# Optimization experiments

Measured on AMD Instinct MI355X. Metric: run time of the kernel, lower is better.

## Reference

```python
import jax, jax.numpy as jnp
import numpy as np
from jax import lax

# dims: B batch, V views, D feature dim, C classes, P prompts
B, V, D, C, P = 512, 10, 1024, 100, 4
ADAPTER_RATIO = 0.6
EPS = 0.01          # sinkhorn entropic regularizer (compute_logits default)
MAX_ITER = 1000     # compute_logits default
THRESH = 1e-2       # PLOT Sinkhorn early-stop threshold on |r - r_prev|.mean()
BN_EPS = 1e-5


def setup_inputs() -> dict:
    key = jax.random.key(0)
    ks = jax.random.split(key, 8)
    # Correlated features so cosine similarity ~0.9 (realistic CLIP-like sims);
    # keeps exp(-wdist/0.01) well inside fp32 range for the Sinkhorn solver.
    base = jax.random.normal(ks[0], (D,), jnp.float32)
    feat = base[None, :] + 0.3 * jax.random.normal(ks[1], (B * V, D), jnp.float32)
    text_feat = base[None, None, :] + 0.3 * jax.random.normal(ks[2], (C, P, D), jnp.float32)
    w = lambda k, shp: 0.02 * jax.random.normal(k, shp, jnp.float32)
    return {
        "feat": feat,                       # (B*V, D) CLIP visual features
        "text_feat": text_feat,             # (C, P, D) encoded text features
        "fusion_ratio": jnp.full((V,), 0.5, jnp.float32),
        "bn1_gamma": jnp.ones((D,), jnp.float32),
        "bn1_beta": jnp.zeros((D,), jnp.float32),
        "W_glob": w(ks[3], (D, D * V)),     # Linear(D*V -> D), torch layout (out, in)
        "b_glob": jnp.zeros((D,), jnp.float32),
        "bn2_gamma": jnp.ones((D,), jnp.float32),
        "bn2_beta": jnp.zeros((D,), jnp.float32),
        "W_v1": w(ks[4], (D, D)),           # Linear(D -> D)
        "b_v1": jnp.zeros((D,), jnp.float32),
        "W_v2": w(ks[5], (D * V, D)),       # Linear(D -> D*V)
        "b_v2": jnp.zeros((D * V,), jnp.float32),
        "logit_scale": jnp.array(np.log(1.0 / 0.07), jnp.float32),
    }


def _bn_train(x, gamma, beta):
    # BatchNorm1d in training mode: biased batch statistics over axis 0
    m = x.mean(axis=0)
    v = x.var(axis=0)
    return (x - m) * lax.rsqrt(v + BN_EPS) * gamma + beta


def _adapter(feat, fusion_ratio, bn1_g, bn1_b, Wg, bg, bn2_g, bn2_b, Wv1, bv1, Wv2, bv2):
    img = feat.reshape(-1, V, D)
    res = feat.reshape(-1, V * D)
    x = img * fusion_ratio.reshape(1, -1, 1)          # per-view fusion weights
    x = _bn_train(x.reshape(-1, D), bn1_g, bn1_b)     # BatchNormPoint over D
    x = x.reshape(-1, V * D)                          # Flatten
    g = jax.nn.relu(_bn_train(x @ Wg.T + bg, bn2_g, bn2_b))   # global_f (dropout=0)
    view = jax.nn.relu(jax.nn.relu(g @ Wv1.T + bv1) @ Wv2.T + bv2)  # view_f
    return view * ADAPTER_RATIO + res * (1.0 - ADAPTER_RATIO)


def _sinkhorn(K, p, q):
    # PLOT-style Sinkhorn: r = p / (K c); c = q / (K^T r); early stop on mean |dr|
    r0 = jnp.ones_like(p)
    c0 = jnp.ones_like(q)

    def cond(st):
        i, r, c, err = st
        return jnp.logical_and(i < MAX_ITER, err > THRESH)

    def body(st):
        i, r, c, _ = st
        r_prev = r
        r = p / jnp.einsum('nvp,np->nv', K, c)
        c = q / jnp.einsum('nvp,nv->np', K, r)
        err = jnp.mean(jnp.abs(r - r_prev))
        return i + 1, r, c, err

    _, r, c, _ = lax.while_loop(cond, body, (jnp.int32(0), r0, c0, jnp.float32(jnp.inf)))
    return r[:, :, None] * K * c[:, None, :]   # T = diag(r) K diag(c)


def reference(feat, text_feat, fusion_ratio, bn1_gamma, bn1_beta, W_glob, b_glob,
              bn2_gamma, bn2_beta, W_v1, b_v1, W_v2, b_v2, logit_scale):
    img_feat = _adapter(feat, fusion_ratio, bn1_gamma, bn1_beta, W_glob, b_glob,
                        bn2_gamma, bn2_beta, W_v1, b_v1, W_v2, b_v2)
    img_feat = img_feat.reshape(-1, V, D)
    img_feat = img_feat / jnp.linalg.norm(img_feat, axis=-1, keepdims=True)
    txt = text_feat / jnp.linalg.norm(text_feat, axis=-1, keepdims=True)

    # compute_logits: sim (B, C, V, P) -> (B*C, V, P)
    sim = jnp.einsum('bvd,cpd->bcvp', img_feat, txt).reshape(B * C, V, P)
    wdist = 1.0 - sim
    p = jnp.full((B * C, V), 1.0 / V, sim.dtype)
    q = jnp.full((B * C, P), 1.0 / P, sim.dtype)
    K = jnp.exp(-wdist / EPS)
    T = _sinkhorn(lax.stop_gradient(K), p, q)   # solver runs under no_grad
    d_OT = jnp.sum(T * wdist, axis=(1, 2)).reshape(B, C)
    logits = jnp.exp(logit_scale) * (1.0 - d_OT)
    return logits
```

## Files before the change

### kernel.cpp

```cpp
#include <hip/hip_runtime.h>
#include <cstdint>


typedef unsigned short u16;
typedef __attribute__((ext_vector_type(8))) short bf8v;
typedef __attribute__((ext_vector_type(4))) float f4v;

__device__ __forceinline__ float4 ld4(const float* p){ return *reinterpret_cast<const float4*>(p); }
__device__ __forceinline__ void st4(float* p, float4 v){ *reinterpret_cast<float4*>(p) = v; }
__device__ __forceinline__ u16 f2bf(float x){
  uint32_t u = __float_as_uint(x);
  return (u16)((u + 0x7FFFu + ((u>>16)&1u)) >> 16);
}
__device__ __forceinline__ uint32_t pk(float a, float b){
  return (uint32_t)f2bf(a) | ((uint32_t)f2bf(b)<<16);
}
__device__ __forceinline__ void glds16(const u16* g, u16* l){
  __builtin_amdgcn_global_load_lds(
      (const __attribute__((address_space(1))) unsigned int*)g,
      (__attribute__((address_space(3))) unsigned int*)l, 16, 0, 0);
}

__device__ __forceinline__ void remap(int map, int NBX, int NBY,
                                      int& bx, int& by, int& bz)
{
  if (map == 0){ bx = blockIdx.x; by = blockIdx.y; bz = blockIdx.z; return; }
  const int i = blockIdx.x, xcd = i & 7, j = i >> 3;
  if (map == 1){
    const int mnC = NBX*NBY;
    const int zPer = (gridDim.x >> 3) / mnC;
    bz = xcd*zPer + j/mnC;
    const int mn = j % mnC; bx = mn % NBX; by = mn / NBX;
  } else {
    const int nbxPer = NBX >> 3;
    bx = xcd*nbxPer + j % nbxPer; by = j / nbxPer; bz = 0;
  }
}

__global__ __launch_bounds__(256,4)
void gemm_bf16_nt(const u16* __restrict__ A, const u16* __restrict__ B,
                  float* __restrict__ C, int lda, int ldb, int ldc,
                  int kLen, long strideCz, int map, int NBX, int NBY)
{
  __shared__ u16 As0[2048], Bs0[4096], As1[2048], Bs1[4096];
  const int tid = threadIdx.x, lane = tid & 63, w = tid >> 6;
  int bx, by, bz; remap(map, NBX, NBY, bx, by, bz);

  const long bm = (long)by*64, bn = (long)bx*128;
  const long kz = (long)bz*kLen;
  C += (long)bz*strideCz;

  const int srow  = lane>>2;
  const int sslot = (lane&3) ^ ((lane>>3)&3);
  const u16* Ag = A + (bm + w*16 + srow)*(long)lda + kz + sslot*8;
  const u16* Bg = B + (bn + w*32 + srow)*(long)ldb + kz + sslot*8;
  const long b16 = 16L*ldb;
  const int woffA = w*512, woffB = w*1024;

  const int fr = lane & 15;
  const int rslot = ((lane>>4) ^ ((lane>>1)&3))*16;
  const int wr = (w>>1)*32, wc = (w&1)*64;

  const f4v zero = {0.f,0.f,0.f,0.f};
  f4v acc[2][4];
  #pragma unroll
  for (int i2=0;i2<2;i2++)
    #pragma unroll
    for (int j2=0;j2<4;j2++) acc[i2][j2]=zero;

  auto STAGE = [&](u16* Al, u16* Bl, int kt){
    glds16(Ag + kt,       Al + woffA);
    glds16(Bg + kt,       Bl + woffB);
    glds16(Bg + kt + b16, Bl + woffB + 512);
  };
  auto COMPUTE = [&](const u16* Asb, const u16* Bsb){
    bf8v af[2], bf[4];
    #pragma unroll
    for (int mi=0; mi<2; ++mi)
      af[mi] = *(const bf8v*)((const char*)Asb + (wr+mi*16+fr)*64 + rslot);
    #pragma unroll
    for (int nj=0; nj<4; ++nj)
      bf[nj] = *(const bf8v*)((const char*)Bsb + (wc+nj*16+fr)*64 + rslot);
    #pragma unroll
    for (int mi=0; mi<2; ++mi)
      #pragma unroll
      for (int nj=0; nj<4; ++nj)
        acc[mi][nj] = __builtin_amdgcn_mfma_f32_16x16x32_bf16(af[mi], bf[nj], acc[mi][nj], 0,0,0);
  };

  STAGE(As0, Bs0, 0);
  __syncthreads();
  int kt = 32;
  for (; kt < kLen - 32; kt += 64){
    STAGE(As1, Bs1, kt);
    COMPUTE(As0, Bs0);
    __syncthreads();
    STAGE(As0, Bs0, kt + 32);
    COMPUTE(As1, Bs1);
    __syncthreads();
  }
  STAGE(As1, Bs1, kt);
  COMPUTE(As0, Bs0);
  __syncthreads();
  COMPUTE(As1, Bs1);

  const int orow = (lane>>4)*4;
  #pragma unroll
  for (int mi=0;mi<2;++mi){
    #pragma unroll
    for (int q=0;q<4;++q){
      const long row = bm + wr + mi*16 + orow + q;
      float* Crow = C + row*(long)ldc + bn + wc + fr;
      #pragma unroll
      for (int nj=0;nj<4;++nj) Crow[nj*16] = acc[mi][nj][q];
    }
  }
}

__global__ __launch_bounds__(256)
void cvt_w(const float* __restrict__ Wg, const float* __restrict__ Wv1,
           u16* __restrict__ WB, u16* __restrict__ W1b)
{
  const long NG = 1310720;
  const long NT = NG + 131072;
  for (long i = (long)blockIdx.x*256 + threadIdx.x; i < NT; i += (long)gridDim.x*256){
    const float* src; u16* dst; long k;
    if (i < NG){ src = Wg; dst = WB; k = i; }
    else       { src = Wv1; dst = W1b; k = i - NG; }
    const float4 a = ld4(&src[k*8]), b = ld4(&src[k*8+4]);
    uint4 o;
    o.x = pk(a.x,a.y); o.y = pk(a.z,a.w);
    o.z = pk(b.x,b.y); o.w = pk(b.z,b.w);
    *reinterpret_cast<uint4*>(&dst[k*8]) = o;
  }
}

__global__ __launch_bounds__(256)
void cvt_bf16(const float* __restrict__ in, u16* __restrict__ out, long n8)
{
  for (long i = (long)blockIdx.x*256 + threadIdx.x; i < n8; i += (long)gridDim.x*256){
    const float4 a = ld4(&in[i*8]), b = ld4(&in[i*8+4]);
    uint4 o;
    o.x = pk(a.x,a.y); o.y = pk(a.z,a.w);
    o.z = pk(b.x,b.y); o.w = pk(b.z,b.w);
    *reinterpret_cast<uint4*>(&out[i*8]) = o;
  }
}

__global__ __launch_bounds__(256)
void reduce_f32_stats(const float* __restrict__ P, int S, int MN,
                      const float* __restrict__ bias, float* __restrict__ out,
                      float* __restrict__ part)
{
  const int b = blockIdx.x, t = threadIdx.x;
  const long i = (long)b*1024 + t*4;
  float4 s = ld4(&P[i]);
  for (int z=1; z<S; ++z){
    const float4 v = ld4(&P[(long)z*MN + i]);
    s.x+=v.x; s.y+=v.y; s.z+=v.z; s.w+=v.w;
  }
  const float4 bb = ld4(&bias[t*4]);
  s.x+=bb.x; s.y+=bb.y; s.z+=bb.z; s.w+=bb.w;
  st4(&out[i], s);
  float* p = part + (long)b*2048;
  st4(&p[t*4], s);
  st4(&p[1024+t*4], make_float4(s.x*s.x, s.y*s.y, s.z*s.z, s.w*s.w));
}

__global__ __launch_bounds__(256)
void reduce_bf16(const float* __restrict__ P, int S, int MN,
                 const float* __restrict__ bias, u16* __restrict__ out)
{
  const long i = ((long)blockIdx.x*256 + threadIdx.x)*4;
  float4 s = ld4(&P[i]);
  for (int z=1; z<S; ++z){
    const float4 v = ld4(&P[(long)z*MN + i]);
    s.x+=v.x; s.y+=v.y; s.z+=v.z; s.w+=v.w;
  }
  const float4 b = ld4(&bias[(int)(i & 1023)]);
  s.x = fmaxf(s.x+b.x,0.f); s.y = fmaxf(s.y+b.y,0.f);
  s.z = fmaxf(s.z+b.z,0.f); s.w = fmaxf(s.w+b.w,0.f);
  uint2 o; o.x = pk(s.x,s.y); o.y = pk(s.z,s.w);
  *reinterpret_cast<uint2*>(&out[i]) = o;
}

__global__ __launch_bounds__(256)
void colstats_p1(const float* __restrict__ X, int rpb, const float* __restrict__ fr,
                 float* __restrict__ part)
{
  const int c = threadIdx.x*4;
  const long r0 = (long)blockIdx.x*rpb;
  float4 s = make_float4(0,0,0,0), q = make_float4(0,0,0,0);
  for (int rr=0; rr<rpb; ++rr){
    const long r = r0+rr;
    float4 x = ld4(&X[r*1024 + c]);
    if (fr){ const float f = fr[(int)(r%10)]; x.x*=f; x.y*=f; x.z*=f; x.w*=f; }
    s.x+=x.x; s.y+=x.y; s.z+=x.z; s.w+=x.w;
    q.x+=x.x*x.x; q.y+=x.y*x.y; q.z+=x.z*x.z; q.w+=x.w*x.w;
  }
  float* p = part + (long)blockIdx.x*2048;
  st4(&p[c], s);
  st4(&p[1024+c], q);
}

__global__ __launch_bounds__(256)
void colstats_reduce(const float* __restrict__ in, float* __restrict__ out,
                     int nslab, int chunk)
{
  const int idx = blockIdx.x*256 + threadIdx.x;
  const int s0 = blockIdx.y*chunk;
  const int s1 = min(nslab, s0+chunk);
  float a0=0.f, a1=0.f, a2=0.f, a3=0.f;
  int s = s0;
  for (; s+4 <= s1; s += 4){
    a0 += in[(long)s*2048+idx];
    a1 += in[(long)(s+1)*2048+idx];
    a2 += in[(long)(s+2)*2048+idx];
    a3 += in[(long)(s+3)*2048+idx];
  }
  for (; s < s1; ++s) a0 += in[(long)s*2048+idx];
  out[(long)blockIdx.y*2048 + idx] = (a0+a1)+(a2+a3);
}

__global__ __launch_bounds__(256)
void bn_apply_bf16(const float* __restrict__ X, const float* __restrict__ fr,
                   const float* __restrict__ stats, float invN,
                   const float* __restrict__ gamma,
                   const float* __restrict__ beta, int relu, u16* __restrict__ out)
{
  const long i = ((long)blockIdx.x*256 + threadIdx.x)*4;
  const int d = (int)(i & 1023);
  const float4 s  = ld4(&stats[d]);
  const float4 qq = ld4(&stats[1024+d]);
  const float4 gm = ld4(&gamma[d]);
  const float4 bt = ld4(&beta[d]);
  float4 sc, sh;
  { const float m=s.x*invN, v=qq.x*invN-m*m; sc.x=gm.x*rsqrtf(v+1e-5f); sh.x=bt.x-m*sc.x; }
  { const float m=s.y*invN, v=qq.y*invN-m*m; sc.y=gm.y*rsqrtf(v+1e-5f); sh.y=bt.y-m*sc.y; }
  { const float m=s.z*invN, v=qq.z*invN-m*m; sc.z=gm.z*rsqrtf(v+1e-5f); sh.z=bt.z-m*sc.z; }
  { const float m=s.w*invN, v=qq.w*invN-m*m; sc.w=gm.w*rsqrtf(v+1e-5f); sh.w=bt.w-m*sc.w; }
  float4 x = ld4(&X[i]);
  if (fr){ const float f = fr[(int)((i>>10)%10)]; x.x*=f; x.y*=f; x.z*=f; x.w*=f; }
  x.x = x.x*sc.x + sh.x; x.y = x.y*sc.y + sh.y;
  x.z = x.z*sc.z + sh.z; x.w = x.w*sc.w + sh.w;
  if (relu){ x.x=fmaxf(x.x,0.f); x.y=fmaxf(x.y,0.f); x.z=fmaxf(x.z,0.f); x.w=fmaxf(x.w,0.f); }
  uint2 o; o.x = pk(x.x,x.y); o.y = pk(x.z,x.w);
  *reinterpret_cast<uint2*>(&out[i]) = o;
}

__device__ __forceinline__ float blockSum256(float v, float* sh4){
  #pragma unroll
  for (int m=32; m; m>>=1) v += __shfl_xor(v, m, 64);
  const int w = threadIdx.x >> 6;
  if ((threadIdx.x & 63) == 0) sh4[w] = v;
  __syncthreads();
  return sh4[0]+sh4[1]+sh4[2]+sh4[3];
}

__global__ __launch_bounds__(256)
void rownorm_bf16(const float* __restrict__ X, u16* __restrict__ out)
{
  __shared__ float sh4[4];
  const int row = blockIdx.x;
  const int d = threadIdx.x*4;
  if (row >= 400){ *reinterpret_cast<uint2*>(&out[(long)row*1024 + d]) = make_uint2(0,0); return; }
  const long base = (long)row*1024 + d;
  const float4 x = ld4(&X[base]);
  const float ss = x.x*x.x + x.y*x.y + x.z*x.z + x.w*x.w;
  const float rn = rsqrtf(blockSum256(ss, sh4));
  uint2 o; o.x = pk(x.x*rn, x.y*rn); o.y = pk(x.z*rn, x.w*rn);
  *reinterpret_cast<uint2*>(&out[base]) = o;
}

__global__ __launch_bounds__(256)
void mix_norm_bf16(const float* __restrict__ P, const float* __restrict__ feat,
                   const float* __restrict__ bv2, u16* __restrict__ outp)
{
  __shared__ float sh4[4];
  const int m = blockIdx.x;
  const int v = m % 10;
  const long base = (long)m*1024;
  const int d = threadIdx.x*4;
  const float4 y  = ld4(&P[base+d]);
  const float4 bb = ld4(&bv2[v*1024 + d]);
  const float4 f  = ld4(&feat[base+d]);
  float4 img;
  img.x = 0.6f*fmaxf(y.x+bb.x,0.f) + 0.4f*f.x;
  img.y = 0.6f*fmaxf(y.y+bb.y,0.f) + 0.4f*f.y;
  img.z = 0.6f*fmaxf(y.z+bb.z,0.f) + 0.4f*f.z;
  img.w = 0.6f*fmaxf(y.w+bb.w,0.f) + 0.4f*f.w;
  const float ss = img.x*img.x + img.y*img.y + img.z*img.z + img.w*img.w;
  const float rn = rsqrtf(blockSum256(ss, sh4));
  uint2 o; o.x = pk(img.x*rn, img.y*rn); o.y = pk(img.z*rn, img.w*rn);
  *reinterpret_cast<uint2*>(&outp[base+d]) = o;
}

__global__ __launch_bounds__(64)
void sinkhorn_solve(const float* __restrict__ sim, const float* __restrict__ lsp,
                    float* __restrict__ out)
{
  const int n = blockIdx.x*64 + threadIdx.x;
  const int b = n / 100, c = n % 100;
  float S[10][4], Km[10][4];
  #pragma unroll
  for (int v=0; v<10; ++v){
    const long off = (long)(b*10+v)*512 + c*4;
    const float4 a0 = ld4(&sim[off]);
    const float4 a1 = ld4(&sim[2621440L + off]);
    S[v][0]=a0.x+a1.x; S[v][1]=a0.y+a1.y; S[v][2]=a0.z+a1.z; S[v][3]=a0.w+a1.w;
    #pragma unroll
    for (int p=0;p<4;++p) Km[v][p] = expf((S[v][p]-1.f)*100.f);
  }
  float r[10], cc[4];
  #pragma unroll
  for (int v=0;v<10;++v) r[v]=1.f;
  #pragma unroll
  for (int p=0;p<4;++p) cc[p]=1.f;
  for (int j=0; j<1000; ++j){
    float lerr = 0.f;
    #pragma unroll
    for (int v=0;v<10;++v){
      const float s = Km[v][0]*cc[0]+Km[v][1]*cc[1]+Km[v][2]*cc[2]+Km[v][3]*cc[3];
      const float rn = __fdividef(0.1f, s);
      lerr += fabsf(rn - r[v]); r[v]=rn;
    }
    #pragma unroll
    for (int p=0;p<4;++p){
      float s = 0.f;
      #pragma unroll
      for (int v=0;v<10;++v) s += Km[v][p]*r[v];
      cc[p] = __fdividef(0.25f, s);
    }
    if (j & 1){
      float w = lerr;
      #pragma unroll
      for (int m=32; m; m>>=1) w += __shfl_xor(w, m, 64);
      if (w <= 0.25f) break;
    }
  }
  float dOT = 0.f;
  #pragma unroll
  for (int v=0;v<10;++v)
    #pragma unroll
    for (int p=0;p<4;++p)
      dOT += r[v]*Km[v][p]*cc[p]*(1.f - S[v][p]);
  out[n] = expf(lsp[0]) * (1.f - dOT);
}

extern "C" void kernel_launch(void* const* d_in, const int* in_sizes, int n_in,
                              void* d_out, int out_size, void* d_ws, size_t ws_size,
                              hipStream_t stream)
{
  const float* feat  = (const float*)d_in[0];
  const float* textf = (const float*)d_in[1];
  const float* fr    = (const float*)d_in[2];
  const float* bn1g  = (const float*)d_in[3];
  const float* bn1b  = (const float*)d_in[4];
  const float* Wg    = (const float*)d_in[5];
  const float* bg    = (const float*)d_in[6];
  const float* bn2g  = (const float*)d_in[7];
  const float* bn2b  = (const float*)d_in[8];
  const float* Wv1   = (const float*)d_in[9];
  const float* bv1   = (const float*)d_in[10];
  const float* Wv2   = (const float*)d_in[11];
  const float* bv2   = (const float*)d_in[12];
  const float* ls    = (const float*)d_in[13];
  float* out = (float*)d_out;
  char* base = (char*)d_ws;

  u16*   WB  = (u16*)(base + 0);
  u16*   Xb  = (u16*)(base + 20971520);
  float* P   = (float*)(base + 31457280);
  float* P2  = P + 1310720;
  u16*   W1b = (u16*)(base + 65011712);
  float* y1  = (float*)(base + 67108864);
  u16*   Gb  = (u16*)(base + 69206016);
  u16*   Hb  = (u16*)(base + 70254592);
  u16*   Tb  = (u16*)(base + 71303168);
  float* ex  = (float*)(base + 72351744);
  float* bn1st=ex, *bn2st=ex+2048;
  float* partY = ex + 4096;
  float* partY2= partY + 1048576;

  cvt_w<<<2048,256,0,stream>>>(Wg, Wv1, WB, W1b);

  colstats_p1<<<640,256,0,stream>>>(feat, 8, fr, P);
  colstats_reduce<<<dim3(8,20),256,0,stream>>>(P, P2, 640, 32);
  colstats_reduce<<<dim3(8,1),256,0,stream>>>(P2, bn1st, 20, 20);
  bn_apply_bf16<<<5120,256,0,stream>>>(feat, fr, bn1st, 1.f/5120.f,
                                       bn1g, bn1b, 0, Xb);

  gemm_bf16_nt<<<1024,256,0,stream>>>(Xb, WB, P, 10240,10240,1024, 640,
                                      524288L, 1, 8, 8);
  reduce_f32_stats<<<512,256,0,stream>>>(P, 16, 524288, bg, y1, partY);
  colstats_reduce<<<dim3(8,16),256,0,stream>>>(partY, partY2, 512, 32);
  colstats_reduce<<<dim3(8,1),256,0,stream>>>(partY2, bn2st, 16, 16);
  bn_apply_bf16<<<512,256,0,stream>>>(y1, nullptr, bn2st, 1.f/512.f,
                                      bn2g, bn2b, 1, Gb);

  gemm_bf16_nt<<<512,256,0,stream>>>(Gb, W1b, P, 1024,1024,1024, 128,
                                     524288L, 1, 8, 8);
  reduce_bf16<<<512,256,0,stream>>>(P, 8, 524288, bv1, Hb);

  cvt_bf16<<<2048,256,0,stream>>>(Wv2, WB, 1310720);

  gemm_bf16_nt<<<640,256,0,stream>>>(Hb, WB, P, 1024,1024,10240, 1024, 0L,
                                     2, 80, 8);
  mix_norm_bf16<<<5120,256,0,stream>>>(P, feat, bv2, Xb);

  rownorm_bf16<<<512,256,0,stream>>>(textf, Tb);
  gemm_bf16_nt<<<dim3(4,80,2),256,0,stream>>>(Xb, Tb, P, 1024,1024,512, 512,
                                              2621440L, 0, 0, 0);

  sinkhorn_solve<<<800,64,0,stream>>>(P, ls, out);
}
```

Baseline: 154.1 us.

## Fuse bias-relu epilogue into GEMM, fold stats reduction, halve split-K

The third GEMM now applies bias, ReLU and the 0.6 scale in its epilogue and writes bf16 directly, so mix_norm reads half the bytes and skips the bias load. The final stat reduction passes are removed by having bn_apply sum 8 partial slabs itself. The big first GEMM's split-K factor drops from 16 to 8, which halves partial-output traffic and the reduce work but also halves grid parallelism. Together these cut several launches and intermediate round-trips. The cost is a little per-thread redundant summation and extra rounding of the intermediate to bf16.

Measured after the change: 167.3 us. +8.6%, slower.

```diff
diff --git a/kernel.cpp b/kernel.cpp
--- a/kernel.cpp
+++ b/kernel.cpp
@@ -12,6 +12,7 @@
   uint32_t u = __float_as_uint(x);
   return (u16)((u + 0x7FFFu + ((u>>16)&1u)) >> 16);
 }
+__device__ __forceinline__ float bf2f(u16 h){ return __uint_as_float(((uint32_t)h)<<16); }
 __device__ __forceinline__ uint32_t pk(float a, float b){
   return (uint32_t)f2bf(a) | ((uint32_t)f2bf(b)<<16);
 }
@@ -40,7 +41,8 @@
 __global__ __launch_bounds__(256,4)
 void gemm_bf16_nt(const u16* __restrict__ A, const u16* __restrict__ B,
                   float* __restrict__ C, int lda, int ldb, int ldc,
-                  int kLen, long strideCz, int map, int NBX, int NBY)
+                  int kLen, long strideCz, int map, int NBX, int NBY,
+                  u16* __restrict__ OB, const float* __restrict__ bv2r)
 {
   __shared__ u16 As0[2048], Bs0[4096], As1[2048], Bs1[4096];
   const int tid = threadIdx.x, lane = tid & 63, w = tid >> 6;
@@ -105,14 +107,31 @@
   COMPUTE(As1, Bs1);
 
   const int orow = (lane>>4)*4;
-  #pragma unroll
-  for (int mi=0;mi<2;++mi){
-    #pragma unroll
-    for (int q=0;q<4;++q){
-      const long row = bm + wr + mi*16 + orow + q;
-      float* Crow = C + row*(long)ldc + bn + wc + fr;
+  if (OB){
+    float bv[4];
+    #pragma unroll
+    for (int nj=0;nj<4;++nj) bv[nj] = bv2r[bn + wc + fr + nj*16];
+    #pragma unroll
+    for (int mi=0;mi<2;++mi){
       #pragma unroll
-      for (int nj=0;nj<4;++nj) Crow[nj*16] = acc[mi][nj][q];
+      for (int q=0;q<4;++q){
+        const long row = bm + wr + mi*16 + orow + q;
+        u16* Orow = OB + row*(long)ldc + bn + wc + fr;
+        #pragma unroll
+        for (int nj=0;nj<4;++nj)
+          Orow[nj*16] = f2bf(0.6f*fmaxf(acc[mi][nj][q] + bv[nj], 0.f));
+      }
+    }
+  } else {
+    #pragma unroll
+    for (int mi=0;mi<2;++mi){
+      #pragma unroll
+      for (int q=0;q<4;++q){
+        const long row = bm + wr + mi*16 + orow + q;
+        float* Crow = C + row*(long)ldc + bn + wc + fr;
+        #pragma unroll
+        for (int nj=0;nj<4;++nj) Crow[nj*16] = acc[mi][nj][q];
+      }
     }
   }
 }
@@ -224,14 +243,19 @@
 
 __global__ __launch_bounds__(256)
 void bn_apply_bf16(const float* __restrict__ X, const float* __restrict__ fr,
-                   const float* __restrict__ stats, float invN,
+                   const float* __restrict__ part, int nslab, float invN,
                    const float* __restrict__ gamma,
                    const float* __restrict__ beta, int relu, u16* __restrict__ out)
 {
   const long i = ((long)blockIdx.x*256 + threadIdx.x)*4;
   const int d = (int)(i & 1023);
-  const float4 s  = ld4(&stats[d]);
-  const float4 qq = ld4(&stats[1024+d]);
+  float4 s = make_float4(0,0,0,0), qq = make_float4(0,0,0,0);
+  for (int sl=0; sl<nslab; ++sl){
+    const float4 a = ld4(&part[(long)sl*2048 + d]);
+    const float4 b = ld4(&part[(long)sl*2048 + 1024 + d]);
+    s.x+=a.x; s.y+=a.y; s.z+=a.z; s.w+=a.w;
+    qq.x+=b.x; qq.y+=b.y; qq.z+=b.z; qq.w+=b.w;
+  }
   const float4 gm = ld4(&gamma[d]);
   const float4 bt = ld4(&beta[d]);
   float4 sc, sh;
@@ -273,22 +297,20 @@
 }
 
 __global__ __launch_bounds__(256)
-void mix_norm_bf16(const float* __restrict__ P, const float* __restrict__ feat,
-                   const float* __restrict__ bv2, u16* __restrict__ outp)
+void mix_norm_bf16(const u16* __restrict__ T3, const float* __restrict__ feat,
+                   u16* __restrict__ outp)
 {
   __shared__ float sh4[4];
   const int m = blockIdx.x;
-  const int v = m % 10;
   const long base = (long)m*1024;
   const int d = threadIdx.x*4;
-  const float4 y  = ld4(&P[base+d]);
-  const float4 bb = ld4(&bv2[v*1024 + d]);
+  const uint2 tv = *reinterpret_cast<const uint2*>(&T3[base+d]);
   const float4 f  = ld4(&feat[base+d]);
   float4 img;
-  img.x = 0.6f*fmaxf(y.x+bb.x,0.f) + 0.4f*f.x;
-  img.y = 0.6f*fmaxf(y.y+bb.y,0.f) + 0.4f*f.y;
-  img.z = 0.6f*fmaxf(y.z+bb.z,0.f) + 0.4f*f.z;
-  img.w = 0.6f*fmaxf(y.w+bb.w,0.f) + 0.4f*f.w;
+  img.x = bf2f((u16)(tv.x&0xffff))   + 0.4f*f.x;
+  img.y = bf2f((u16)(tv.x>>16))      + 0.4f*f.y;
+  img.z = bf2f((u16)(tv.y&0xffff))   + 0.4f*f.z;
+  img.w = bf2f((u16)(tv.y>>16))      + 0.4f*f.w;
   const float ss = img.x*img.x + img.y*img.y + img.z*img.z + img.w*img.w;
   const float rn = rsqrtf(blockSum256(ss, sh4));
   uint2 o; o.x = pk(img.x*rn, img.y*rn); o.y = pk(img.z*rn, img.w*rn);
@@ -378,39 +400,36 @@
   u16*   Hb  = (u16*)(base + 70254592);
   u16*   Tb  = (u16*)(base + 71303168);
   float* ex  = (float*)(base + 72351744);
-  float* bn1st=ex, *bn2st=ex+2048;
   float* partY = ex + 4096;
   float* partY2= partY + 1048576;
 
   cvt_w<<<2048,256,0,stream>>>(Wg, Wv1, WB, W1b);
 
   colstats_p1<<<640,256,0,stream>>>(feat, 8, fr, P);
-  colstats_reduce<<<dim3(8,20),256,0,stream>>>(P, P2, 640, 32);
-  colstats_reduce<<<dim3(8,1),256,0,stream>>>(P2, bn1st, 20, 20);
-  bn_apply_bf16<<<5120,256,0,stream>>>(feat, fr, bn1st, 1.f/5120.f,
+  colstats_reduce<<<dim3(8,8),256,0,stream>>>(P, P2, 640, 80);
+  bn_apply_bf16<<<5120,256,0,stream>>>(feat, fr, P2, 8, 1.f/5120.f,
                                        bn1g, bn1b, 0, Xb);
 
-  gemm_bf16_nt<<<1024,256,0,stream>>>(Xb, WB, P, 10240,10240,1024, 640,
-                                      524288L, 1, 8, 8);
-  reduce_f32_stats<<<512,256,0,stream>>>(P, 16, 524288, bg, y1, partY);
-  colstats_reduce<<<dim3(8,16),256,0,stream>>>(partY, partY2, 512, 32);
-  colstats_reduce<<<dim3(8,1),256,0,stream>>>(partY2, bn2st, 16, 16);
-  bn_apply_bf16<<<512,256,0,stream>>>(y1, nullptr, bn2st, 1.f/512.f,
+  gemm_bf16_nt<<<512,256,0,stream>>>(Xb, WB, P, 10240,10240,1024, 1280,
+                                     524288L, 1, 8, 8, nullptr, nullptr);
+  reduce_f32_stats<<<512,256,0,stream>>>(P, 8, 524288, bg, y1, partY);
+  colstats_reduce<<<dim3(8,8),256,0,stream>>>(partY, partY2, 512, 64);
+  bn_apply_bf16<<<512,256,0,stream>>>(y1, nullptr, partY2, 8, 1.f/512.f,
                                       bn2g, bn2b, 1, Gb);
 
   gemm_bf16_nt<<<512,256,0,stream>>>(Gb, W1b, P, 1024,1024,1024, 128,
-                                     524288L, 1, 8, 8);
+                                     524288L, 1, 8, 8, nullptr, nullptr);
   reduce_bf16<<<512,256,0,stream>>>(P, 8, 524288, bv1, Hb);
 
   cvt_bf16<<<2048,256,0,stream>>>(Wv2, WB, 1310720);
 
-  gemm_bf16_nt<<<640,256,0,stream>>>(Hb, WB, P, 1024,1024,10240, 1024, 0L,
-                                     2, 80, 8);
-  mix_norm_bf16<<<5120,256,0,stream>>>(P, feat, bv2, Xb);
+  gemm_bf16_nt<<<640,256,0,stream>>>(Hb, WB, nullptr, 1024,1024,10240, 1024,
+                                     0L, 2, 80, 8, (u16*)P, bv2);
+  mix_norm_bf16<<<5120,256,0,stream>>>((u16*)P, feat, Xb);
 
   rownorm_bf16<<<512,256,0,stream>>>(textf, Tb);
   gemm_bf16_nt<<<dim3(4,80,2),256,0,stream>>>(Xb, Tb, P, 1024,1024,512, 512,
-                                              2621440L, 0, 0, 0);
+                                              2621440L, 0, 0, 0, nullptr, nullptr);
 
   sinkhorn_solve<<<800,64,0,stream>>>(P, ls, out);
 }
```
